# Performance work log

Measured on AMD Instinct MI355X. Metric: run time of the kernel, lower is better.

The kernel has to match this reference:

```python
import jax, jax.numpy as jnp
import numpy as np

EMBED_DIM = 1024
NUM_HEADS = 16
HEAD_DIM = EMBED_DIM // NUM_HEADS


def setup_inputs() -> dict:
    key = jax.random.key(0)
    ks = jax.random.split(key, 11)
    B, S, E = 4, 2048, EMBED_DIM
    s = 1.0 / np.sqrt(E)
    return {
        "query": jax.random.normal(ks[0], (B, S, E), jnp.float32),
        "key": jax.random.normal(ks[1], (B, S, E), jnp.float32),
        "value": jax.random.normal(ks[2], (B, S, E), jnp.float32),
        "Wq": jax.random.normal(ks[3], (E, E), jnp.float32) * s,
        "bq": jnp.zeros((E,), jnp.float32),
        "Wk": jax.random.normal(ks[4], (E, E), jnp.float32) * s,
        "bk": jnp.zeros((E,), jnp.float32),
        "Wv": jax.random.normal(ks[5], (E, E), jnp.float32) * s,
        "bv": jnp.zeros((E,), jnp.float32),
        "Wo": jax.random.normal(ks[6], (E, E), jnp.float32) * s,
        "bo": jnp.zeros((E,), jnp.float32),
    }


def reference(query, key, value, Wq, bq, Wk, bk, Wv, bv, Wo, bo):
    B, S, E = query.shape
    H, D = NUM_HEADS, HEAD_DIM
    scale = jnp.float32(np.sqrt(D))
    # linear projections (torch Linear: x @ W.T + b)
    Q = (query @ Wq.T + bq).reshape(B, S, H, D).transpose(0, 2, 1, 3)  # [B,H,S,D]
    K = (key @ Wk.T + bk).reshape(B, S, H, D).transpose(0, 2, 1, 3)
    V = (value @ Wv.T + bv).reshape(B, S, H, D).transpose(0, 2, 1, 3)
    # full O(S^2) score materialization, matching the eager torch code
    scores = jnp.einsum("bhqd,bhkd->bhqk", Q, K) / scale  # [B,H,S,S]
    attn = jax.nn.softmax(scores, axis=-1)
    out = jnp.einsum("bhqk,bhkd->bhqd", attn, V)  # [B,H,S,D]
    out = out.transpose(0, 2, 1, 3).reshape(B, S, E)
    out = out @ Wo.T + bo
    return out, attn.mean(axis=1)
```

## Files before the change

### kernel.cpp

```cpp
#include <hip/hip_runtime.h>
#include <hip/hip_bf16.h>

#define DEVI __device__ __forceinline__

typedef __bf16 bf16x8 __attribute__((ext_vector_type(8)));
typedef __bf16 bf16x4 __attribute__((ext_vector_type(4)));
typedef float f32x4 __attribute__((ext_vector_type(4)));

constexpr int B_ = 4, S_ = 2048, E_ = 1024, H_ = 16, D_ = 64;
constexpr int N_ = B_ * S_;
constexpr float SCALE_ = 0.125f;

constexpr size_t XB_OFF = 0;
constexpr size_t WB_OFF = 50331648;
constexpr size_t QB_OFF = 58720256;
constexpr size_t KB_OFF = 75497472;
constexpr size_t VT_OFF = 92274688;
constexpr size_t CTX_OFF = 109051904;
constexpr size_t LS_OFF = 125829120;
constexpr size_t WS_NEED = 126353408;

typedef const __attribute__((address_space(1))) void* gas_ptr;
typedef __attribute__((address_space(3))) void* las_ptr;

DEVI void load_lds16(const void* g, void* l) {
  __builtin_amdgcn_global_load_lds((gas_ptr)g, (las_ptr)l, 16, 0, 0);
}

DEVI f32x4 mfma16(bf16x8 a, bf16x8 b, f32x4 c) {
  return __builtin_amdgcn_mfma_f32_16x16x32_bf16(a, b, c, 0, 0, 0);
}

__global__ __launch_bounds__(256) void conv_x(const float* __restrict__ q,
                                              const float* __restrict__ k,
                                              const float* __restrict__ v,
                                              __bf16* __restrict__ dst) {
  const float* src = (blockIdx.y == 0) ? q : ((blockIdx.y == 1) ? k : v);
  __bf16* d = dst + (size_t)blockIdx.y * N_ * E_;
  size_t i = ((size_t)blockIdx.x * blockDim.x + threadIdx.x) * 4;
  float4 f = *(const float4*)(src + i);
  bf16x4 o;
  o[0] = (__bf16)f.x; o[1] = (__bf16)f.y; o[2] = (__bf16)f.z; o[3] = (__bf16)f.w;
  *(bf16x4*)(d + i) = o;
}

__global__ __launch_bounds__(256) void conv_w(const float* __restrict__ wq,
                                              const float* __restrict__ wk,
                                              const float* __restrict__ wv,
                                              const float* __restrict__ wo,
                                              __bf16* __restrict__ dst) {
  const float* src = (blockIdx.y == 0) ? wq : ((blockIdx.y == 1) ? wk :
                     ((blockIdx.y == 2) ? wv : wo));
  __bf16* d = dst + (size_t)blockIdx.y * E_ * E_;
  size_t i = ((size_t)blockIdx.x * blockDim.x + threadIdx.x) * 4;
  float4 f = *(const float4*)(src + i);
  bf16x4 o;
  o[0] = (__bf16)f.x; o[1] = (__bf16)f.y; o[2] = (__bf16)f.z; o[3] = (__bf16)f.w;
  *(bf16x4*)(d + i) = o;
}

__global__ __launch_bounds__(256) void gemm_qkv(const __bf16* __restrict__ Xb,
                                                const __bf16* __restrict__ Wb,
                                                const float* __restrict__ bq,
                                                const float* __restrict__ bk,
                                                const float* __restrict__ bv,
                                                __bf16* __restrict__ Qb,
                                                __bf16* __restrict__ Kb,
                                                __bf16* __restrict__ Vt) {
  __shared__ __attribute__((aligned(16))) __bf16 As[128 * 32];
  __shared__ __attribute__((aligned(16))) __bf16 Bs[128 * 32];
  const int z = blockIdx.z;
  const __bf16* A = Xb + (size_t)z * N_ * E_;
  const __bf16* W = Wb + (size_t)z * E_ * E_;
  const float* bias = (z == 0) ? bq : ((z == 1) ? bk : bv);
  const int m0 = blockIdx.x * 128, n0 = blockIdx.y * 128;
  const int t = threadIdx.x, lane = t & 63, w = t >> 6;
  const int wm = w >> 1, wn = w & 1;

  f32x4 acc[4][4] = {};

  for (int kk = 0; kk < E_; kk += 32) {
#pragma unroll
    for (int i = 0; i < 2; ++i) {
      int c = t + i * 256;
      int row = c >> 2, kc = c & 3;
      load_lds16(A + (size_t)(m0 + row) * E_ + kk + kc * 8, (void*)(As + c * 8));
      load_lds16(W + (size_t)(n0 + row) * E_ + kk + kc * 8, (void*)(Bs + c * 8));
    }
    __syncthreads();
    bf16x8 a[4], b[4];
#pragma unroll
    for (int i = 0; i < 4; ++i)
      a[i] = *(const bf16x8*)(As + (wm * 64 + i * 16 + (lane & 15)) * 32 + ((lane >> 4) * 8));
#pragma unroll
    for (int j = 0; j < 4; ++j)
      b[j] = *(const bf16x8*)(Bs + (wn * 64 + j * 16 + (lane & 15)) * 32 + ((lane >> 4) * 8));
#pragma unroll
    for (int i = 0; i < 4; ++i)
#pragma unroll
      for (int j = 0; j < 4; ++j)
        acc[i][j] = mfma16(a[i], b[j], acc[i][j]);
    __syncthreads();
  }

#pragma unroll
  for (int i = 0; i < 4; ++i) {
    int mloc = wm * 64 + i * 16 + ((lane >> 4) << 2);
#pragma unroll
    for (int j = 0; j < 4; ++j) {
      int nloc = wn * 64 + j * 16 + (lane & 15);
      int n = n0 + nloc;
      int h = n >> 6, d = n & 63;
      float bs = bias[n];
      if (z == 2) {
        int m = m0 + mloc;
        int bb = m >> 11, s = m & 2047;
        bf16x4 pk;
#pragma unroll
        for (int r = 0; r < 4; ++r) pk[r] = (__bf16)(acc[i][j][r] + bs);
        *(bf16x4*)(Vt + ((size_t)(bb * H_ + h) * D_ + d) * S_ + s) = pk;
      } else {
        __bf16* dst = (z == 0) ? Qb : Kb;
#pragma unroll
        for (int r = 0; r < 4; ++r) {
          int m = m0 + mloc + r;
          int bb = m >> 11, s = m & 2047;
          dst[((size_t)(bb * H_ + h) * S_ + s) * D_ + d] = (__bf16)(acc[i][j][r] + bs);
        }
      }
    }
  }
}

__global__ __launch_bounds__(256) void attn_pv(const __bf16* __restrict__ Qb,
                                               const __bf16* __restrict__ Kb,
                                               const __bf16* __restrict__ Vt,
                                               float* __restrict__ Lsum,
                                               __bf16* __restrict__ Ctx) {
  __shared__ __attribute__((aligned(16))) __bf16 Qs[2 * 128 * 32];
  __shared__ __attribute__((aligned(16))) __bf16 Ks[2 * 64 * 32];
  __shared__ __attribute__((aligned(16))) __bf16 Vs[2 * 64 * 32];
  __shared__ __attribute__((aligned(16))) __bf16 Ps[128 * 72];
  __shared__ float lred[2][128];

  const int q0 = blockIdx.x * 128;
  const int bh = blockIdx.y;
  const __bf16* Qh = Qb + (size_t)bh * S_ * D_;
  const __bf16* Kh = Kb + (size_t)bh * S_ * D_;
  const __bf16* Vh = Vt + (size_t)bh * D_ * S_;
  const int t = threadIdx.x, lane = t & 63, w = t >> 6;
  const int wm = w >> 1, wn = w & 1;

#pragma unroll
  for (int i = 0; i < 4; ++i) {
    int c = t + i * 256;
    int sub = c >> 9, rem = c & 511, row = rem >> 2, kc = rem & 3;
    load_lds16(Qh + (size_t)(q0 + row) * D_ + sub * 32 + kc * 8, (void*)(Qs + c * 8));
  }
  __syncthreads();
  bf16x8 aq[4][2];
#pragma unroll
  for (int i = 0; i < 4; ++i)
#pragma unroll
    for (int ks = 0; ks < 2; ++ks)
      aq[i][ks] = *(const bf16x8*)(Qs + ks * 4096 + (wm * 64 + i * 16 + (lane & 15)) * 32 + ((lane >> 4) * 8));

  f32x4 acc_o[4][2] = {};
  float lacc[4][4] = {};

  for (int k0 = 0; k0 < S_; k0 += 64) {
#pragma unroll
    for (int i = 0; i < 2; ++i) {
      int c = t + i * 256;
      int sub = c >> 8, rem = c & 255, row = rem >> 2, kc = rem & 3;
      load_lds16(Kh + (size_t)(k0 + row) * D_ + sub * 32 + kc * 8, (void*)(Ks + c * 8));
      load_lds16(Vh + (size_t)row * S_ + k0 + sub * 32 + kc * 8, (void*)(Vs + c * 8));
    }
    __syncthreads();

#pragma unroll
    for (int i = 0; i < 4; ++i) {
#pragma unroll
      for (int j = 0; j < 2; ++j) {
        f32x4 s = {};
#pragma unroll
        for (int ks = 0; ks < 2; ++ks) {
          bf16x8 bk_ = *(const bf16x8*)(Ks + ks * 2048 + (wn * 32 + j * 16 + (lane & 15)) * 32 + ((lane >> 4) * 8));
          s = mfma16(aq[i][ks], bk_, s);
        }
        int row = wm * 64 + i * 16 + ((lane >> 4) << 2);
        int col = wn * 32 + j * 16 + (lane & 15);
#pragma unroll
        for (int r = 0; r < 4; ++r) {
          float e = __expf(s[r] * SCALE_);
          lacc[i][r] += e;
          Ps[(row + r) * 72 + col] = (__bf16)e;
        }
      }
    }
    __syncthreads();

#pragma unroll
    for (int ks = 0; ks < 2; ++ks) {
      bf16x8 ap[4];
#pragma unroll
      for (int i = 0; i < 4; ++i)
        ap[i] = *(const bf16x8*)(Ps + (size_t)(wm * 64 + i * 16 + (lane & 15)) * 72 + ks * 32 + ((lane >> 4) * 8));
#pragma unroll
      for (int j = 0; j < 2; ++j) {
        bf16x8 bv_ = *(const bf16x8*)(Vs + ks * 2048 + (wn * 32 + j * 16 + (lane & 15)) * 32 + ((lane >> 4) * 8));
#pragma unroll
        for (int i = 0; i < 4; ++i)
          acc_o[i][j] = mfma16(ap[i], bv_, acc_o[i][j]);
      }
    }
    __syncthreads();
  }

#pragma unroll
  for (int i = 0; i < 4; ++i)
#pragma unroll
    for (int r = 0; r < 4; ++r) {
      float v = lacc[i][r];
      v += __shfl_xor(v, 1);
      v += __shfl_xor(v, 2);
      v += __shfl_xor(v, 4);
      v += __shfl_xor(v, 8);
      if ((lane & 15) == 0)
        lred[wn][wm * 64 + i * 16 + ((lane >> 4) << 2) + r] = v;
    }
  __syncthreads();

  if (t < 128)
    Lsum[(size_t)bh * S_ + q0 + t] = lred[0][t] + lred[1][t];

  const int bb = bh >> 4, h = bh & 15;
#pragma unroll
  for (int i = 0; i < 4; ++i) {
    int rowb = wm * 64 + i * 16 + ((lane >> 4) << 2);
#pragma unroll
    for (int r = 0; r < 4; ++r) {
      float invl = 1.0f / (lred[0][rowb + r] + lred[1][rowb + r]);
      int q = q0 + rowb + r;
#pragma unroll
      for (int j = 0; j < 2; ++j) {
        int d = wn * 32 + j * 16 + (lane & 15);
        Ctx[((size_t)bb * S_ + q) * E_ + h * 64 + d] = (__bf16)(acc_o[i][j][r] * invl);
      }
    }
  }
}

__global__ __launch_bounds__(256) void attn_mean(const __bf16* __restrict__ Qb,
                                                 const __bf16* __restrict__ Kb,
                                                 const float* __restrict__ Lsum,
                                                 float* __restrict__ meanout) {
  __shared__ __attribute__((aligned(16))) __bf16 Qs[2 * 128 * 32];
  __shared__ __attribute__((aligned(16))) __bf16 Ks2[2 * 128 * 32];
  __shared__ float Lt[128];
  const int k0 = blockIdx.x * 128, q0 = blockIdx.y * 128, bI = blockIdx.z;
  const int t = threadIdx.x, lane = t & 63, w = t >> 6;
  const int wm = w >> 1, wn = w & 1;

  float macc[4][4][4] = {};

  for (int h = 0; h < H_; ++h) {
    const size_t bh = (size_t)bI * H_ + h;
    const __bf16* Qh = Qb + bh * S_ * D_;
    const __bf16* Kh = Kb + bh * S_ * D_;
#pragma unroll
    for (int i = 0; i < 4; ++i) {
      int c = t + i * 256;
      int sub = c >> 9, rem = c & 511, row = rem >> 2, kc = rem & 3;
      load_lds16(Qh + (size_t)(q0 + row) * D_ + sub * 32 + kc * 8, (void*)(Qs + c * 8));
      load_lds16(Kh + (size_t)(k0 + row) * D_ + sub * 32 + kc * 8, (void*)(Ks2 + c * 8));
    }
    if (t < 128) Lt[t] = 1.0f / Lsum[bh * S_ + q0 + t];
    __syncthreads();

    bf16x8 a[4][2], bb[4][2];
#pragma unroll
    for (int i = 0; i < 4; ++i)
#pragma unroll
      for (int ks = 0; ks < 2; ++ks)
        a[i][ks] = *(const bf16x8*)(Qs + ks * 4096 + (wm * 64 + i * 16 + (lane & 15)) * 32 + ((lane >> 4) * 8));
#pragma unroll
    for (int j = 0; j < 4; ++j)
#pragma unroll
      for (int ks = 0; ks < 2; ++ks)
        bb[j][ks] = *(const bf16x8*)(Ks2 + ks * 4096 + (wn * 64 + j * 16 + (lane & 15)) * 32 + ((lane >> 4) * 8));

    float invl[4][4];
#pragma unroll
    for (int i = 0; i < 4; ++i) {
      int rowb = wm * 64 + i * 16 + ((lane >> 4) << 2);
#pragma unroll
      for (int r = 0; r < 4; ++r) invl[i][r] = Lt[rowb + r];
    }

#pragma unroll
    for (int i = 0; i < 4; ++i)
#pragma unroll
      for (int j = 0; j < 4; ++j) {
        f32x4 s = {};
#pragma unroll
        for (int ks = 0; ks < 2; ++ks) s = mfma16(a[i][ks], bb[j][ks], s);
#pragma unroll
        for (int r = 0; r < 4; ++r)
          macc[i][j][r] += __expf(s[r] * SCALE_) * invl[i][r];
      }
    __syncthreads();
  }

#pragma unroll
  for (int i = 0; i < 4; ++i) {
    int rowb = wm * 64 + i * 16 + ((lane >> 4) << 2);
#pragma unroll
    for (int j = 0; j < 4; ++j) {
      int col = k0 + wn * 64 + j * 16 + (lane & 15);
#pragma unroll
      for (int r = 0; r < 4; ++r)
        meanout[((size_t)bI * S_ + q0 + rowb + r) * S_ + col] = macc[i][j][r] * 0.0625f;
    }
  }
}

__global__ __launch_bounds__(256) void gemm_out(const __bf16* __restrict__ Ctx,
                                                const __bf16* __restrict__ Wo,
                                                const float* __restrict__ bo,
                                                float* __restrict__ out) {
  __shared__ __attribute__((aligned(16))) __bf16 As[128 * 32];
  __shared__ __attribute__((aligned(16))) __bf16 Bs[128 * 32];
  const int m0 = blockIdx.x * 128, n0 = blockIdx.y * 128;
  const int t = threadIdx.x, lane = t & 63, w = t >> 6;
  const int wm = w >> 1, wn = w & 1;

  f32x4 acc[4][4] = {};

  for (int kk = 0; kk < E_; kk += 32) {
#pragma unroll
    for (int i = 0; i < 2; ++i) {
      int c = t + i * 256;
      int row = c >> 2, kc = c & 3;
      load_lds16(Ctx + (size_t)(m0 + row) * E_ + kk + kc * 8, (void*)(As + c * 8));
      load_lds16(Wo + (size_t)(n0 + row) * E_ + kk + kc * 8, (void*)(Bs + c * 8));
    }
    __syncthreads();
    bf16x8 a[4], b[4];
#pragma unroll
    for (int i = 0; i < 4; ++i)
      a[i] = *(const bf16x8*)(As + (wm * 64 + i * 16 + (lane & 15)) * 32 + ((lane >> 4) * 8));
#pragma unroll
    for (int j = 0; j < 4; ++j)
      b[j] = *(const bf16x8*)(Bs + (wn * 64 + j * 16 + (lane & 15)) * 32 + ((lane >> 4) * 8));
#pragma unroll
    for (int i = 0; i < 4; ++i)
#pragma unroll
      for (int j = 0; j < 4; ++j)
        acc[i][j] = mfma16(a[i], b[j], acc[i][j]);
    __syncthreads();
  }

#pragma unroll
  for (int i = 0; i < 4; ++i) {
    int mloc = wm * 64 + i * 16 + ((lane >> 4) << 2);
#pragma unroll
    for (int j = 0; j < 4; ++j) {
      int n = n0 + wn * 64 + j * 16 + (lane & 15);
      float bs = bo[n];
#pragma unroll
      for (int r = 0; r < 4; ++r)
        out[(size_t)(m0 + mloc + r) * E_ + n] = acc[i][j][r] + bs;
    }
  }
}

extern "C" void kernel_launch(void* const* d_in, const int* in_sizes, int n_in,
                              void* d_out, int out_size, void* d_ws, size_t ws_size,
                              hipStream_t stream) {
  if (ws_size < WS_NEED) {
    hipMemsetAsync(d_out, 0, (size_t)out_size * sizeof(float), stream);
    return;
  }

  const float* q  = (const float*)d_in[0];
  const float* k  = (const float*)d_in[1];
  const float* v  = (const float*)d_in[2];
  const float* Wq = (const float*)d_in[3];
  const float* bq = (const float*)d_in[4];
  const float* Wk = (const float*)d_in[5];
  const float* bk = (const float*)d_in[6];
  const float* Wv = (const float*)d_in[7];
  const float* bv = (const float*)d_in[8];
  const float* Wo = (const float*)d_in[9];
  const float* bo = (const float*)d_in[10];

  char* ws = (char*)d_ws;
  __bf16* Xb  = (__bf16*)(ws + XB_OFF);
  __bf16* Wb  = (__bf16*)(ws + WB_OFF);
  __bf16* Qb  = (__bf16*)(ws + QB_OFF);
  __bf16* Kb  = (__bf16*)(ws + KB_OFF);
  __bf16* Vt  = (__bf16*)(ws + VT_OFF);
  __bf16* Ctx = (__bf16*)(ws + CTX_OFF);
  float*  Ls  = (float*)(ws + LS_OFF);

  float* out0 = (float*)d_out;
  float* out1 = (float*)d_out + (size_t)N_ * E_;

  conv_x<<<dim3(N_ * E_ / 4 / 256, 3), 256, 0, stream>>>(q, k, v, Xb);
  conv_w<<<dim3(E_ * E_ / 4 / 256, 4), 256, 0, stream>>>(Wq, Wk, Wv, Wo, Wb);
  gemm_qkv<<<dim3(N_ / 128, E_ / 128, 3), 256, 0, stream>>>(Xb, Wb, bq, bk, bv, Qb, Kb, Vt);
  attn_pv<<<dim3(S_ / 128, B_ * H_), 256, 0, stream>>>(Qb, Kb, Vt, Ls, Ctx);
  attn_mean<<<dim3(S_ / 128, S_ / 128, B_), 256, 0, stream>>>(Qb, Kb, Ls, out1);
  gemm_out<<<dim3(N_ / 128, E_ / 128), 256, 0, stream>>>(Ctx, Wb + 3 * (size_t)E_ * E_, bo, out0);
}
```

Baseline: 500.6 us.

## Compute transposed scores in registers, drop LDS round-trip for P and row sums

```diff
diff --git a/kernel.cpp b/kernel.cpp
--- a/kernel.cpp
+++ b/kernel.cpp
@@ -132,16 +132,14 @@
   }
 }
 
-__global__ __launch_bounds__(256) void attn_pv(const __bf16* __restrict__ Qb,
-                                               const __bf16* __restrict__ Kb,
-                                               const __bf16* __restrict__ Vt,
-                                               float* __restrict__ Lsum,
-                                               __bf16* __restrict__ Ctx) {
+__global__ __launch_bounds__(256, 4) void attn_pv(const __bf16* __restrict__ Qb,
+                                                  const __bf16* __restrict__ Kb,
+                                                  const __bf16* __restrict__ Vt,
+                                                  float* __restrict__ Lsum,
+                                                  __bf16* __restrict__ Ctx) {
   __shared__ __attribute__((aligned(16))) __bf16 Qs[2 * 128 * 32];
   __shared__ __attribute__((aligned(16))) __bf16 Ks[2 * 64 * 32];
   __shared__ __attribute__((aligned(16))) __bf16 Vs[2 * 64 * 32];
-  __shared__ __attribute__((aligned(16))) __bf16 Ps[128 * 72];
-  __shared__ float lred[2][128];
 
   const int q0 = blockIdx.x * 128;
   const int bh = blockIdx.y;
@@ -149,7 +147,8 @@
   const __bf16* Kh = Kb + (size_t)bh * S_ * D_;
   const __bf16* Vh = Vt + (size_t)bh * D_ * S_;
   const int t = threadIdx.x, lane = t & 63, w = t >> 6;
-  const int wm = w >> 1, wn = w & 1;
+  const int l15 = lane & 15, ghi8 = (lane >> 4) * 8;
+  const int ksel = 8 * (l15 >> 2) + (l15 & 3);
 
 #pragma unroll
   for (int i = 0; i < 4; ++i) {
@@ -158,15 +157,19 @@
     load_lds16(Qh + (size_t)(q0 + row) * D_ + sub * 32 + kc * 8, (void*)(Qs + c * 8));
   }
   __syncthreads();
-  bf16x8 aq[4][2];
-#pragma unroll
-  for (int i = 0; i < 4; ++i)
+  bf16x8 qf[2][2];
+#pragma unroll
+  for (int jb = 0; jb < 2; ++jb)
 #pragma unroll
     for (int ks = 0; ks < 2; ++ks)
-      aq[i][ks] = *(const bf16x8*)(Qs + ks * 4096 + (wm * 64 + i * 16 + (lane & 15)) * 32 + ((lane >> 4) * 8));
-
-  f32x4 acc_o[4][2] = {};
-  float lacc[4][4] = {};
+      qf[jb][ks] = *(const bf16x8*)(Qs + ks * 4096 + (w * 32 + jb * 16 + l15) * 32 + ghi8);
+
+  bf16x8 ones;
+#pragma unroll
+  for (int i = 0; i < 8; ++i) ones[i] = (__bf16)1.0f;
+
+  f32x4 acc[4][2] = {};
+  f32x4 lacc[2] = {};
 
   for (int k0 = 0; k0 < S_; k0 += 64) {
 #pragma unroll
@@ -179,90 +182,76 @@
     __syncthreads();
 
 #pragma unroll
-    for (int i = 0; i < 4; ++i) {
-#pragma unroll
-      for (int j = 0; j < 2; ++j) {
-        f32x4 s = {};
-#pragma unroll
-        for (int ks = 0; ks < 2; ++ks) {
-          bf16x8 bk_ = *(const bf16x8*)(Ks + ks * 2048 + (wn * 32 + j * 16 + (lane & 15)) * 32 + ((lane >> 4) * 8));
-          s = mfma16(aq[i][ks], bk_, s);
+    for (int chunk = 0; chunk < 2; ++chunk) {
+      f32x4 sc[2][2];
+#pragma unroll
+      for (int blk = 0; blk < 2; ++blk) {
+        int krow = chunk * 32 + 4 * blk + ksel;
+        bf16x8 kf0 = *(const bf16x8*)(Ks + krow * 32 + ghi8);
+        bf16x8 kf1 = *(const bf16x8*)(Ks + 2048 + krow * 32 + ghi8);
+#pragma unroll
+        for (int jb = 0; jb < 2; ++jb) {
+          f32x4 s = {};
+          s = mfma16(kf0, qf[jb][0], s);
+          s = mfma16(kf1, qf[jb][1], s);
+          sc[blk][jb] = s;
         }
-        int row = wm * 64 + i * 16 + ((lane >> 4) << 2);
-        int col = wn * 32 + j * 16 + (lane & 15);
+      }
+      bf16x8 pf[2];
+#pragma unroll
+      for (int jb = 0; jb < 2; ++jb) {
 #pragma unroll
         for (int r = 0; r < 4; ++r) {
-          float e = __expf(s[r] * SCALE_);
-          lacc[i][r] += e;
-          Ps[(row + r) * 72 + col] = (__bf16)e;
+          pf[jb][r]     = (__bf16)__expf(sc[0][jb][r] * SCALE_);
+          pf[jb][4 + r] = (__bf16)__expf(sc[1][jb][r] * SCALE_);
         }
-      }
-    }
-    __syncthreads();
-
-#pragma unroll
-    for (int ks = 0; ks < 2; ++ks) {
-      bf16x8 ap[4];
-#pragma unroll
-      for (int i = 0; i < 4; ++i)
-        ap[i] = *(const bf16x8*)(Ps + (size_t)(wm * 64 + i * 16 + (lane & 15)) * 72 + ks * 32 + ((lane >> 4) * 8));
-#pragma unroll
-      for (int j = 0; j < 2; ++j) {
-        bf16x8 bv_ = *(const bf16x8*)(Vs + ks * 2048 + (wn * 32 + j * 16 + (lane & 15)) * 32 + ((lane >> 4) * 8));
-#pragma unroll
-        for (int i = 0; i < 4; ++i)
-          acc_o[i][j] = mfma16(ap[i], bv_, acc_o[i][j]);
-      }
-    }
-    __syncthreads();
-  }
-
-#pragma unroll
-  for (int i = 0; i < 4; ++i)
-#pragma unroll
-    for (int r = 0; r < 4; ++r) {
-      float v = lacc[i][r];
-      v += __shfl_xor(v, 1);
-      v += __shfl_xor(v, 2);
-      v += __shfl_xor(v, 4);
-      v += __shfl_xor(v, 8);
-      if ((lane & 15) == 0)
-        lred[wn][wm * 64 + i * 16 + ((lane >> 4) << 2) + r] = v;
-    }
-  __syncthreads();
-
-  if (t < 128)
-    Lsum[(size_t)bh * S_ + q0 + t] = lred[0][t] + lred[1][t];
+        lacc[jb] = mfma16(ones, pf[jb], lacc[jb]);
+      }
+#pragma unroll
+      for (int mb = 0; mb < 4; ++mb) {
+        bf16x8 vf = *(const bf16x8*)(Vs + chunk * 2048 + (mb * 16 + l15) * 32 + ghi8);
+#pragma unroll
+        for (int jb = 0; jb < 2; ++jb)
+          acc[mb][jb] = mfma16(vf, pf[jb], acc[mb][jb]);
+      }
+    }
+    __syncthreads();
+  }
+
+  if (lane < 16) {
+#pragma unroll
+    for (int jb = 0; jb < 2; ++jb)
+      Lsum[(size_t)bh * S_ + q0 + w * 32 + jb * 16 + lane] = lacc[jb][0];
+  }
 
   const int bb = bh >> 4, h = bh & 15;
 #pragma unroll
-  for (int i = 0; i < 4; ++i) {
-    int rowb = wm * 64 + i * 16 + ((lane >> 4) << 2);
-#pragma unroll
-    for (int r = 0; r < 4; ++r) {
-      float invl = 1.0f / (lred[0][rowb + r] + lred[1][rowb + r]);
-      int q = q0 + rowb + r;
-#pragma unroll
-      for (int j = 0; j < 2; ++j) {
-        int d = wn * 32 + j * 16 + (lane & 15);
-        Ctx[((size_t)bb * S_ + q) * E_ + h * 64 + d] = (__bf16)(acc_o[i][j][r] * invl);
-      }
-    }
-  }
-}
-
-__global__ __launch_bounds__(256) void attn_mean(const __bf16* __restrict__ Qb,
-                                                 const __bf16* __restrict__ Kb,
-                                                 const float* __restrict__ Lsum,
-                                                 float* __restrict__ meanout) {
+  for (int jb = 0; jb < 2; ++jb) {
+    float invl = 1.0f / lacc[jb][0];
+    int q = q0 + w * 32 + jb * 16 + l15;
+#pragma unroll
+    for (int mb = 0; mb < 4; ++mb) {
+      int d = mb * 16 + ((lane >> 4) << 2);
+      bf16x4 pk;
+#pragma unroll
+      for (int r = 0; r < 4; ++r) pk[r] = (__bf16)(acc[mb][jb][r] * invl);
+      *(bf16x4*)(Ctx + ((size_t)bb * S_ + q) * E_ + h * 64 + d) = pk;
+    }
+  }
+}
+
+__global__ __launch_bounds__(256, 4) void attn_mean(const __bf16* __restrict__ Qb,
+                                                    const __bf16* __restrict__ Kb,
+                                                    const float* __restrict__ Lsum,
+                                                    float* __restrict__ meanout) {
   __shared__ __attribute__((aligned(16))) __bf16 Qs[2 * 128 * 32];
   __shared__ __attribute__((aligned(16))) __bf16 Ks2[2 * 128 * 32];
-  __shared__ float Lt[128];
   const int k0 = blockIdx.x * 128, q0 = blockIdx.y * 128, bI = blockIdx.z;
   const int t = threadIdx.x, lane = t & 63, w = t >> 6;
-  const int wm = w >> 1, wn = w & 1;
-
-  float macc[4][4][4] = {};
+  const int l15 = lane & 15, ghi8 = (lane >> 4) * 8;
+  const int ksel = 8 * (l15 >> 2) + (l15 & 3);
+
+  f32x4 macc[4][2][2] = {};
 
   for (int h = 0; h < H_; ++h) {
     const size_t bh = (size_t)bI * H_ + h;
@@ -275,54 +264,53 @@
       load_lds16(Qh + (size_t)(q0 + row) * D_ + sub * 32 + kc * 8, (void*)(Qs + c * 8));
       load_lds16(Kh + (size_t)(k0 + row) * D_ + sub * 32 + kc * 8, (void*)(Ks2 + c * 8));
     }
-    if (t < 128) Lt[t] = 1.0f / Lsum[bh * S_ + q0 + t];
-    __syncthreads();
-
-    bf16x8 a[4][2], bb[4][2];
-#pragma unroll
-    for (int i = 0; i < 4; ++i)
+    float invl[2];
+#pragma unroll
+    for (int jb = 0; jb < 2; ++jb)
+      invl[jb] = 1.0f / Lsum[bh * S_ + q0 + w * 32 + jb * 16 + l15];
+    __syncthreads();
+
+    bf16x8 qf[2][2];
+#pragma unroll
+    for (int jb = 0; jb < 2; ++jb)
 #pragma unroll
       for (int ks = 0; ks < 2; ++ks)
-        a[i][ks] = *(const bf16x8*)(Qs + ks * 4096 + (wm * 64 + i * 16 + (lane & 15)) * 32 + ((lane >> 4) * 8));
-#pragma unroll
-    for (int j = 0; j < 4; ++j)
-#pragma unroll
-      for (int ks = 0; ks < 2; ++ks)
-        bb[j][ks] = *(const bf16x8*)(Ks2 + ks * 4096 + (wn * 64 + j * 16 + (lane & 15)) * 32 + ((lane >> 4) * 8));
-
-    float invl[4][4];
-#pragma unroll
-    for (int i = 0; i < 4; ++i) {
-      int rowb = wm * 64 + i * 16 + ((lane >> 4) << 2);
-#pragma unroll
-      for (int r = 0; r < 4; ++r) invl[i][r] = Lt[rowb + r];
-    }
-
-#pragma unroll
-    for (int i = 0; i < 4; ++i)
-#pragma unroll
-      for (int j = 0; j < 4; ++j) {
-        f32x4 s = {};
-#pragma unroll
-        for (int ks = 0; ks < 2; ++ks) s = mfma16(a[i][ks], bb[j][ks], s);
-#pragma unroll
-        for (int r = 0; r < 4; ++r)
-          macc[i][j][r] += __expf(s[r] * SCALE_) * invl[i][r];
-      }
-    __syncthreads();
-  }
-
-#pragma unroll
-  for (int i = 0; i < 4; ++i) {
-    int rowb = wm * 64 + i * 16 + ((lane >> 4) << 2);
-#pragma unroll
-    for (int j = 0; j < 4; ++j) {
-      int col = k0 + wn * 64 + j * 16 + (lane & 15);
-#pragma unroll
-      for (int r = 0; r < 4; ++r)
-        meanout[((size_t)bI * S_ + q0 + rowb + r) * S_ + col] = macc[i][j][r] * 0.0625f;
-    }
-  }
+        qf[jb][ks] = *(const bf16x8*)(Qs + ks * 4096 + (w * 32 + jb * 16 + l15) * 32 + ghi8);
+
+#pragma unroll
+    for (int chunk = 0; chunk < 4; ++chunk) {
+#pragma unroll
+      for (int blk = 0; blk < 2; ++blk) {
+        int krow = chunk * 32 + 4 * blk + ksel;
+        bf16x8 kf0 = *(const bf16x8*)(Ks2 + krow * 32 + ghi8);
+        bf16x8 kf1 = *(const bf16x8*)(Ks2 + 4096 + krow * 32 + ghi8);
+#pragma unroll
+        for (int jb = 0; jb < 2; ++jb) {
+          f32x4 s = {};
+          s = mfma16(kf0, qf[jb][0], s);
+          s = mfma16(kf1, qf[jb][1], s);
+#pragma unroll
+          for (int r = 0; r < 4; ++r)
+            macc[chunk][blk][jb][r] += __expf(s[r] * SCALE_) * invl[jb];
+        }
+      }
+    }
+    __syncthreads();
+  }
+
+#pragma unroll
+  for (int chunk = 0; chunk < 4; ++chunk)
+#pragma unroll
+    for (int blk = 0; blk < 2; ++blk)
+#pragma unroll
+      for (int jb = 0; jb < 2; ++jb) {
+        int q = q0 + w * 32 + jb * 16 + l15;
+        int kb = k0 + chunk * 32 + 8 * (lane >> 4) + 4 * blk;
+        f32x4 o;
+#pragma unroll
+        for (int r = 0; r < 4; ++r) o[r] = macc[chunk][blk][jb][r] * 0.0625f;
+        *(f32x4*)(meanout + ((size_t)bI * S_ + q) * S_ + kb) = o;
+      }
 }
 
 __global__ __launch_bounds__(256) void gemm_out(const __bf16* __restrict__ Ctx,
```

Result: faster. 439.3 us (-12.3%).
